# Kernel optimization log

Hardware: AMD Instinct MI355X
Metric: run time of the kernel (lower is better)

Reference implementation:

```python
import jax, jax.numpy as jnp
import numpy as np

B = 16
NS = [2048, 1024, 512, 256]
K = 12
GROUPS = 64
OUT = 1024
EPS = 1e-5


def setup_inputs() -> dict:
    key = jax.random.key(0)
    ks = iter(jax.random.split(key, 40))
    d = {}
    for i, n in enumerate(NS):
        d[f"fs{i}"] = jax.random.normal(next(ks), (B, n, 256), jnp.float32)
        d[f"xs{i}"] = jax.random.normal(next(ks), (B, n, 3), jnp.float32)
        ct = 1024 if i == 0 else 256
        d[f"ft{i}"] = jax.random.normal(next(ks), (B, n, ct), jnp.float32)
        d[f"xt{i}"] = jax.random.normal(next(ks), (B, n, 3), jnp.float32)
    d["Ws"] = jax.random.normal(next(ks), (4, OUT, 256), jnp.float32) * 0.05
    d["bWs"] = jax.random.normal(next(ks), (4, OUT), jnp.float32) * 0.05
    d["gs"] = jax.random.uniform(next(ks), (4, OUT), jnp.float32, 0.5, 1.5)
    d["bes"] = jax.random.normal(next(ks), (4, OUT), jnp.float32) * 0.05
    d["mus"] = jax.random.normal(next(ks), (4, OUT), jnp.float32) * 0.05
    d["vs"] = jax.random.uniform(next(ks), (4, OUT), jnp.float32, 0.5, 1.5)
    d["Wt0"] = jax.random.normal(next(ks), (OUT, 1024), jnp.float32) * 0.02
    d["Wt123"] = jax.random.normal(next(ks), (3, OUT, 256), jnp.float32) * 0.05
    d["bWt"] = jax.random.normal(next(ks), (4, OUT), jnp.float32) * 0.05
    d["gt"] = jax.random.uniform(next(ks), (4, OUT), jnp.float32, 0.5, 1.5)
    d["bet"] = jax.random.normal(next(ks), (4, OUT), jnp.float32) * 0.05
    d["mut"] = jax.random.normal(next(ks), (4, OUT), jnp.float32) * 0.05
    d["vt"] = jax.random.uniform(next(ks), (4, OUT), jnp.float32, 0.5, 1.5)
    return d


def fps(xyz, m):
    # furthest point sampling starting from index 0 (as in pointnet2_utils)
    b, n, _ = xyz.shape
    idxs = jnp.zeros((b, m), jnp.int32)
    d2 = jnp.full((b, n), 1e10, xyz.dtype)
    last = jnp.zeros((b,), jnp.int32)

    def body(i, st):
        idxs, d2, last = st
        lx = jnp.take_along_axis(xyz, last[:, None, None], axis=1)  # [b,1,3]
        d = jnp.sum((xyz - lx) ** 2, axis=-1)  # [b,n]
        d2 = jnp.minimum(d2, d)
        nxt = jnp.argmax(d2, axis=-1).astype(jnp.int32)
        return idxs.at[:, i].set(nxt), d2, nxt

    idxs, _, _ = jax.lax.fori_loop(1, m, body, (idxs, d2, last))
    return idxs


def gather_points(feat, idx):
    # feat [b,n,c], idx [b,...] -> [b,...,c]
    flat = idx.reshape(idx.shape[0], -1)
    out = jnp.take_along_axis(feat, flat[..., None], axis=1)
    return out.reshape(idx.shape + (feat.shape[-1],))


def knn_point(k, xyz, query):
    # squared pairwise distances [b,m,n]; k smallest (== torch.topk largest=False)
    d = (jnp.sum(query ** 2, -1, keepdims=True)
         - 2.0 * jnp.einsum('bmd,bnd->bmn', query, xyz)
         + jnp.sum(xyz ** 2, -1)[:, None, :])
    _, idx = jax.lax.top_k(-d, k)
    return idx.astype(jnp.int32)


def graph_op(grouped, w, b, g, be, mu, v):
    # grouped [B,M,K,C]; kernel-1 Conv1d == channel matmul; eval-mode BN; ReLU; max over K
    x = jnp.einsum('bmkc,oc->bmko', grouped, w) + b
    x = (x - mu) * (g * jax.lax.rsqrt(v + EPS)) + be
    x = jax.nn.relu(x)
    return jnp.max(x, axis=2)  # [B,M,O]


def reference(fs0, xs0, ft0, xt0, fs1, xs1, ft1, xt1, fs2, xs2, ft2, xt2,
              fs3, xs3, ft3, xt3, Ws, bWs, gs, bes, mus, vs,
              Wt0, Wt123, bWt, gt, bet, mut, vt):
    fs_list = [fs0, fs1, fs2, fs3]
    xs_list = [xs0, xs1, xs2, xs3]
    ft_list = [ft0, ft1, ft2, ft3]
    xt_list = [xt0, xt1, xt2, xt3]

    fps_idx = fps(xt_list[-1], GROUPS)              # [B,G]
    new_xyz = gather_points(xt_list[-1], fps_idx)   # [B,G,3]

    out_s, out_t = [], []
    for i in range(4):
        idx_t = knn_point(K, xt_list[i], new_xyz)   # [B,G,K]
        grp_t = gather_points(ft_list[i], idx_t)    # [B,G,K,Ct]
        idx_s = knn_point(K, xs_list[i], new_xyz)
        grp_s = gather_points(fs_list[i], idx_s)    # [B,G,K,256]
        wt = Wt0 if i == 0 else Wt123[i - 1]
        out_s.append(graph_op(grp_s, Ws[i], bWs[i], gs[i], bes[i], mus[i], vs[i]))
        out_t.append(graph_op(grp_t, wt, bWt[i], gt[i], bet[i], mut[i], vt[i]))
    return (tuple(out_s), tuple(out_t))
```

## Files before the change

kernel.cpp:

```cpp
#include <hip/hip_runtime.h>
#include <hip/hip_bf16.h>

#define DEVI __device__ __forceinline__

typedef __attribute__((ext_vector_type(8))) short bf16x8;
typedef __attribute__((ext_vector_type(4))) float f32x4;
typedef __attribute__((ext_vector_type(8))) unsigned short us8;
typedef __attribute__((ext_vector_type(4))) float fl4;

DEVI unsigned short f2bf(float f) {
  union { float f; unsigned u; } x; x.f = f;
  unsigned r = (x.u + 0x7fffu + ((x.u >> 16) & 1u)) >> 16;
  return (unsigned short)r;
}

DEVI float fadd3(float a, float b, float c) {
  return __fadd_rn(__fadd_rn(a, b), c);
}

__global__ __launch_bounds__(256) void prep_kernel(
    const float* __restrict__ Ws, const float* __restrict__ Wt0,
    const float* __restrict__ Wt123,
    const float* __restrict__ bWs, const float* __restrict__ gs,
    const float* __restrict__ bes, const float* __restrict__ mus,
    const float* __restrict__ vs,
    const float* __restrict__ bWt, const float* __restrict__ gt,
    const float* __restrict__ bet, const float* __restrict__ mut,
    const float* __restrict__ vt,
    char* __restrict__ wbf, float* __restrict__ bnA,
    float* __restrict__ bnB) {
  const unsigned id = blockIdx.x * 256u + threadIdx.x;
  const unsigned WN = 2883584u;
  if (id < WN) {
    float val; unsigned c, o, k, woffE;
    if (id < 1048576u) {
      c = id >> 18; unsigned rem = id & 262143u;
      o = rem >> 8; k = rem & 255u; val = Ws[id]; woffE = c << 18;
    } else if (id < 2097152u) {
      c = 4u; unsigned rem = id - 1048576u;
      o = rem >> 10; k = rem & 1023u; val = Wt0[rem]; woffE = 1048576u;
    } else {
      unsigned rem = id - 2097152u; unsigned cc = rem >> 18;
      c = 5u + cc; unsigned r2 = rem & 262143u;
      o = r2 >> 8; k = r2 & 255u; val = Wt123[rem];
      woffE = 2097152u + (cc << 18);
    }
    unsigned NKT = (c == 4u) ? 16u : 4u;
    unsigned ntile = o >> 8, op = o & 255u, kt = k >> 6, kl = k & 63u;
    unsigned byteoff = (woffE << 1) + ((ntile * NKT + kt) << 15) +
                       ((op * 128u + kl * 2u) ^ ((op & 7u) << 4));
    *(unsigned short*)(wbf + byteoff) = f2bf(val);
  } else if (id < WN + 8192u) {
    unsigned r = id - WN;
    unsigned c = r >> 10, o = r & 1023u;
    float g, bW, mu, v, be;
    if (c < 4u) { g = gs[r]; bW = bWs[r]; mu = mus[r]; v = vs[r]; be = bes[r]; }
    else {
      unsigned r2 = (c - 4u) * 1024u + o;
      g = gt[r2]; bW = bWt[r2]; mu = mut[r2]; v = vt[r2]; be = bet[r2];
    }
    float A = g / sqrtf(v + 1e-5f);
    float B = (bW - mu) * A + be;
    bnA[r] = A; bnB[r] = B;
  }
}

__global__ __launch_bounds__(64) void fps_kernel(const float* __restrict__ xt3,
                                                 float* __restrict__ newxyz) {
  const int b = blockIdx.x;
  const int t = threadIdx.x;
  const float* P = xt3 + (size_t)b * 256 * 3;
  float px[4], py[4], pz[4], d2[4];
#pragma unroll
  for (int j = 0; j < 4; ++j) {
    int p = t + 64 * j;
    px[j] = P[p * 3 + 0]; py[j] = P[p * 3 + 1]; pz[j] = P[p * 3 + 2];
    d2[j] = 1e10f;
  }
  float* NX = newxyz + (size_t)b * 64 * 3;
  float cx = __shfl(px[0], 0), cy = __shfl(py[0], 0), cz = __shfl(pz[0], 0);
  if (t == 0) { NX[0] = cx; NX[1] = cy; NX[2] = cz; }
  for (int i = 1; i < 64; ++i) {
    float bv = -1.0f; int bi = 0;
#pragma unroll
    for (int j = 0; j < 4; ++j) {
      float dx = __fsub_rn(px[j], cx), dy = __fsub_rn(py[j], cy),
            dz = __fsub_rn(pz[j], cz);
      float d = fadd3(__fmul_rn(dx, dx), __fmul_rn(dy, dy), __fmul_rn(dz, dz));
      d2[j] = fminf(d2[j], d);
      int p = t + 64 * j;
      if (j == 0) { bv = d2[0]; bi = t; }
      else if (d2[j] > bv) { bv = d2[j]; bi = p; }
    }
#pragma unroll
    for (int off = 32; off >= 1; off >>= 1) {
      float ov = __shfl_xor(bv, off);
      int oi = __shfl_xor(bi, off);
      if (ov > bv || (ov == bv && oi < bi)) { bv = ov; bi = oi; }
    }
    int s = bi;
    int owner = s & 63, slot = s >> 6;
    float sx = slot == 0 ? px[0] : slot == 1 ? px[1] : slot == 2 ? px[2] : px[3];
    float sy = slot == 0 ? py[0] : slot == 1 ? py[1] : slot == 2 ? py[2] : py[3];
    float sz = slot == 0 ? pz[0] : slot == 1 ? pz[1] : slot == 2 ? pz[2] : pz[3];
    cx = __shfl(sx, owner); cy = __shfl(sy, owner); cz = __shfl(sz, owner);
    if (t == 0) { NX[i * 3 + 0] = cx; NX[i * 3 + 1] = cy; NX[i * 3 + 2] = cz; }
  }
}

template <int NJ>
DEVI void knn_run(int lane, const float* __restrict__ X, float qx, float qy,
                  float qz, float qq, int* __restrict__ out) {
  float d2[NJ];
#pragma unroll
  for (int j = 0; j < NJ; ++j) {
    int pi = lane + 64 * j;
    float x = X[pi * 3 + 0], y = X[pi * 3 + 1], z = X[pi * 3 + 2];
    float xx = fadd3(__fmul_rn(x, x), __fmul_rn(y, y), __fmul_rn(z, z));
    float dot = fadd3(__fmul_rn(qx, x), __fmul_rn(qy, y), __fmul_rn(qz, z));
    d2[j] = __fadd_rn(__fsub_rn(qq, __fmul_rn(2.0f, dot)), xx);
  }
  for (int kk = 0; kk < 12; ++kk) {
    float bv = d2[0]; int bi = lane;
#pragma unroll
    for (int j = 1; j < NJ; ++j) {
      if (d2[j] < bv) { bv = d2[j]; bi = lane + 64 * j; }
    }
#pragma unroll
    for (int off = 1; off <= 32; off <<= 1) {
      float ov = __shfl_xor(bv, off);
      int oi = __shfl_xor(bi, off);
      if (ov < bv || (ov == bv && oi < bi)) { bv = ov; bi = oi; }
    }
    if (lane == 0) out[kk] = bi;
#pragma unroll
    for (int j = 0; j < NJ; ++j)
      if (bi == lane + 64 * j) d2[j] = 3.4e38f;
  }
}

struct KnnP { const float* xyz[8]; };

__global__ __launch_bounds__(256) void knn_kernel(KnnP p,
                                                  const float* __restrict__ newxyz,
                                                  int* __restrict__ idxbuf) {
  const int q = blockIdx.x * 4 + (threadIdx.x >> 6);
  const int lane = threadIdx.x & 63;
  const int c = q >> 10, b = (q >> 6) & 15, g = q & 63;
  const int n = 2048 >> (c & 3);
  const float* X = p.xyz[c] + (size_t)b * n * 3;
  const float* qp = newxyz + ((size_t)b * 64 + g) * 3;
  float qx = qp[0], qy = qp[1], qz = qp[2];
  float qq = fadd3(__fmul_rn(qx, qx), __fmul_rn(qy, qy), __fmul_rn(qz, qz));
  int* out = idxbuf + (size_t)q * 12;
  switch (c & 3) {
    case 0: knn_run<32>(lane, X, qx, qy, qz, qq, out); break;
    case 1: knn_run<16>(lane, X, qx, qy, qz, qq, out); break;
    case 2: knn_run<8>(lane, X, qx, qy, qz, qq, out); break;
    default: knn_run<4>(lane, X, qx, qy, qz, qq, out); break;
  }
}

struct GatherP {
  const float* feat[8];
  int n[8];
  unsigned base16[9];
  unsigned goffB[8];
  int lsh[8];
  int NKT[8];
};

__global__ __launch_bounds__(256) void gather_kernel(GatherP p,
                                                     const int* __restrict__ idxbuf,
                                                     char* __restrict__ grouped) {
  unsigned id = blockIdx.x * 256u + threadIdx.x;
  if (id >= p.base16[8]) return;
  int c = 0;
#pragma unroll
  for (int j = 1; j < 8; ++j) if (id >= p.base16[j]) c = j;
  unsigned local = id - p.base16[c];
  int lsh = p.lsh[c];
  unsigned r = local >> lsh;
  unsigned k8 = local & ((1u << lsh) - 1u);
  unsigned rowp = r & 255u, mtile = r >> 8, group = r >> 4, kslot = r & 15u;
  unsigned b = group >> 6;
  int ke = (kslot < 12u) ? (int)kslot : 0;
  int pidx = idxbuf[(size_t)c * 12288 + group * 12u + ke];
  int C = (lsh == 7) ? 1024 : 256;
  const float* src = p.feat[c] + ((size_t)b * p.n[c] + pidx) * C + k8 * 8u;
  fl4 v0 = *reinterpret_cast<const fl4*>(src);
  fl4 v1 = *reinterpret_cast<const fl4*>(src + 4);
  us8 ov;
  ov[0] = f2bf(v0[0]); ov[1] = f2bf(v0[1]); ov[2] = f2bf(v0[2]); ov[3] = f2bf(v0[3]);
  ov[4] = f2bf(v1[0]); ov[5] = f2bf(v1[1]); ov[6] = f2bf(v1[2]); ov[7] = f2bf(v1[3]);
  unsigned kt = k8 >> 3, kl8 = k8 & 7u;
  unsigned byteoff = p.goffB[c] + (mtile * (unsigned)p.NKT[c] + kt) * 32768u +
                     ((rowp * 128u + kl8 * 16u) ^ ((rowp & 7u) << 4));
  *reinterpret_cast<us8*>(grouped + byteoff) = ov;
}

struct GemmP {
  unsigned goff[8]; unsigned woff[8]; unsigned outoff[8];
  unsigned bnoff[8]; int K[8];
};

#define GLOAD_LDS16(gsrc, ldsdst)                                              \
  __builtin_amdgcn_global_load_lds(                                            \
      (const __attribute__((address_space(1))) void*)(gsrc),                   \
      (__attribute__((address_space(3))) void*)(ldsdst), 16, 0, 0)

template <int DBUF>
__global__ __launch_bounds__(512, 2) void gemm256_kernel(
    const unsigned short* __restrict__ grouped,
    const unsigned short* __restrict__ wbf, const float* __restrict__ bnA,
    const float* __restrict__ bnB, float* __restrict__ out, GemmP p) {
  extern __shared__ char smem[];
  const int z = blockIdx.z;
  const int NKT = p.K[z] >> 6;
  const char* Ag = (const char*)(grouped + p.goff[z]) +
                   (size_t)blockIdx.y * NKT * 32768;
  const char* Bg = (const char*)(wbf + p.woff[z]) +
                   (size_t)blockIdx.x * NKT * 32768;
  const int tid = threadIdx.x;
  const int lane = tid & 63, wid = tid >> 6;
  const int wr = wid >> 2, wc = wid & 3;

  f32x4 acc[8][4];
#pragma unroll
  for (int m = 0; m < 8; ++m)
#pragma unroll
    for (int n = 0; n < 4; ++n) acc[m][n] = (f32x4){0.f, 0.f, 0.f, 0.f};

  auto stage = [&](int buf, int kt2) {
    char* dstA = smem + buf * 65536;
    const char* srcA = Ag + (size_t)kt2 * 32768;
    const char* srcB = Bg + (size_t)kt2 * 32768;
#pragma unroll
    for (int it = 0; it < 4; ++it)
      GLOAD_LDS16(srcA + (it * 512 + tid) * 16, dstA + (it * 512 + wid * 64) * 16);
#pragma unroll
    for (int it = 0; it < 4; ++it)
      GLOAD_LDS16(srcB + (it * 512 + tid) * 16,
                  dstA + 32768 + (it * 512 + wid * 64) * 16);
  };

  auto compute = [&](int kt) {
    const char* As = smem + (DBUF ? ((kt & 1) * 65536) : 0);
    const char* Bs = As + 32768;
#pragma unroll
    for (int ks = 0; ks < 2; ++ks) {
      bf16x8 af[8], bv[4];
#pragma unroll
      for (int m = 0; m < 8; ++m) {
        int row = wr * 128 + m * 16 + (lane & 15);
        int byte = (row * 128 + ks * 64 + ((lane >> 4) * 16)) ^ ((lane & 7) << 4);
        af[m] = *reinterpret_cast<const bf16x8*>(As + byte);
      }
#pragma unroll
      for (int n = 0; n < 4; ++n) {
        int col = wc * 64 + n * 16 + (lane & 15);
        int byte = (col * 128 + ks * 64 + ((lane >> 4) * 16)) ^ ((lane & 7) << 4);
        bv[n] = *reinterpret_cast<const bf16x8*>(Bs + byte);
      }
#pragma unroll
      for (int m = 0; m < 8; ++m)
#pragma unroll
        for (int n = 0; n < 4; ++n)
          acc[m][n] = __builtin_amdgcn_mfma_f32_16x16x32_bf16(af[m], bv[n],
                                                              acc[m][n], 0, 0, 0);
    }
  };

  stage(0, 0);
  asm volatile("s_waitcnt vmcnt(0)" ::: "memory");
  __syncthreads();
  for (int kt = 0; kt < NKT; ++kt) {
    if (DBUF && kt + 1 < NKT) stage((kt + 1) & 1, kt + 1);
    compute(kt);
    if (DBUF) {
      if (kt + 1 < NKT) {
        asm volatile("s_waitcnt vmcnt(0)" ::: "memory");
        __syncthreads();
      }
    } else if (kt + 1 < NKT) {
      __syncthreads();
      stage(0, kt + 1);
      asm volatile("s_waitcnt vmcnt(0)" ::: "memory");
      __syncthreads();
    }
  }

  const float* bA = bnA + p.bnoff[z];
  const float* bB = bnB + p.bnoff[z];
  float* O = out + (size_t)p.outoff[z];
#pragma unroll
  for (int n = 0; n < 4; ++n) {
    int o = blockIdx.x * 256 + wc * 64 + n * 16 + (lane & 15);
    float sA = bA[o], sB = bB[o];
#pragma unroll
    for (int m = 0; m < 8; ++m) {
      float v = fmaxf(fmaxf(acc[m][n][0], acc[m][n][1]),
                      fmaxf(acc[m][n][2], acc[m][n][3]));
      v = fmaxf(v, __shfl_xor(v, 16));
      v = fmaxf(v, __shfl_xor(v, 32));
      if (lane < 16) {
        int group = blockIdx.y * 16 + wr * 8 + m;
        float val = fmaf(v, sA, sB);
        O[(size_t)group * 1024 + o] = fmaxf(val, 0.f);
      }
    }
  }
}

extern "C" void kernel_launch(void* const* d_in, const int* in_sizes, int n_in,
                              void* d_out, int out_size, void* d_ws,
                              size_t ws_size, hipStream_t stream) {
  (void)in_sizes; (void)n_in; (void)out_size; (void)ws_size;
  const float *fs[4], *xs[4], *ft[4], *xt[4];
  for (int i = 0; i < 4; ++i) {
    fs[i] = (const float*)d_in[4 * i + 0];
    xs[i] = (const float*)d_in[4 * i + 1];
    ft[i] = (const float*)d_in[4 * i + 2];
    xt[i] = (const float*)d_in[4 * i + 3];
  }
  const float* Ws = (const float*)d_in[16];
  const float* bWs = (const float*)d_in[17];
  const float* gs = (const float*)d_in[18];
  const float* bes = (const float*)d_in[19];
  const float* mus = (const float*)d_in[20];
  const float* vs = (const float*)d_in[21];
  const float* Wt0 = (const float*)d_in[22];
  const float* Wt123 = (const float*)d_in[23];
  const float* bWt = (const float*)d_in[24];
  const float* gt = (const float*)d_in[25];
  const float* bet = (const float*)d_in[26];
  const float* mut = (const float*)d_in[27];
  const float* vt = (const float*)d_in[28];

  char* ws = (char*)d_ws;
  float* newxyz = (float*)(ws + 0);
  int* idxbuf = (int*)(ws + 16384);
  float* bnA = (float*)(ws + 409600);
  float* bnB = (float*)(ws + 442368);
  char* wbf = ws + 475136;
  char* grouped = ws + 6242304;

  static const int NSarr[4] = {2048, 1024, 512, 256};
  const unsigned goff[8] = {0u,        4194304u,  8388608u,  12582912u,
                            16777216u, 33554432u, 37748736u, 41943040u};
  const unsigned woff[8] = {0u,       262144u,  524288u,  786432u,
                            1048576u, 2097152u, 2359296u, 2621440u};

  prep_kernel<<<11296, 256, 0, stream>>>(Ws, Wt0, Wt123, bWs, gs, bes, mus, vs,
                                         bWt, gt, bet, mut, vt, wbf, bnA, bnB);
  fps_kernel<<<16, 64, 0, stream>>>(xt[3], newxyz);

  KnnP kp;
  for (int i = 0; i < 4; ++i) {
    kp.xyz[i] = xs[i];
    kp.xyz[4 + i] = xt[i];
  }
  knn_kernel<<<2048, 256, 0, stream>>>(kp, newxyz, idxbuf);

  GatherP gp;
  unsigned cum = 0;
  for (int c = 0; c < 8; ++c) {
    int scale = c & 3;
    int K = (c == 4) ? 1024 : 256;
    gp.feat[c] = (c < 4) ? fs[scale] : ft[scale];
    gp.n[c] = NSarr[scale];
    gp.base16[c] = cum;
    gp.goffB[c] = goff[c] * 2u;
    gp.lsh[c] = (K == 1024) ? 7 : 5;
    gp.NKT[c] = K >> 6;
    cum += 16384u * (unsigned)(K / 8);
  }
  gp.base16[8] = cum;
  gather_kernel<<<(cum + 255u) / 256u, 256, 0, stream>>>(gp, idxbuf, grouped);

  GemmP mp;
  for (int c = 0; c < 8; ++c) {
    mp.goff[c] = goff[c]; mp.woff[c] = woff[c];
    mp.outoff[c] = (unsigned)c * 1048576u;
    mp.bnoff[c] = (unsigned)c * 1024u;
    mp.K[c] = (c == 4) ? 1024 : 256;
  }
  hipError_t attr_ok = hipFuncSetAttribute(
      (const void*)gemm256_kernel<1>,
      hipFuncAttributeMaxDynamicSharedMemorySize, 131072);
  if (attr_ok == hipSuccess) {
    gemm256_kernel<1><<<dim3(4, 64, 8), 512, 131072, stream>>>(
        (const unsigned short*)grouped, (const unsigned short*)wbf, bnA, bnB,
        (float*)d_out, mp);
  } else {
    gemm256_kernel<0><<<dim3(4, 64, 8), 512, 65536, stream>>>(
        (const unsigned short*)grouped, (const unsigned short*)wbf, bnA, bnB,
        (float*)d_out, mp);
  }
}
```

Before: 239.8 us.

## Restructure GEMM into 8-phase pipelined loop with prefetch-two and XCD block remap

```diff
diff --git a/kernel.cpp b/kernel.cpp
--- a/kernel.cpp
+++ b/kernel.cpp
@@ -209,8 +209,169 @@
       (const __attribute__((address_space(1))) void*)(gsrc),                   \
       (__attribute__((address_space(3))) void*)(ldsdst), 16, 0, 0)
 
-template <int DBUF>
-__global__ __launch_bounds__(512, 2) void gemm256_kernel(
+__global__ __launch_bounds__(512, 2) void gemm8p_kernel(
+    const unsigned short* __restrict__ grouped,
+    const unsigned short* __restrict__ wbf, const float* __restrict__ bnA,
+    const float* __restrict__ bnB, float* __restrict__ out, GemmP p) {
+  extern __shared__ char smem[];
+  const int bid = blockIdx.x;
+  const int logical = (bid & 7) * 256 + (bid >> 3);
+  const int z = logical >> 8;
+  const int rem = logical & 255;
+  const int mtile = rem >> 2, ntile = rem & 3;
+  const int NKT = p.K[z] >> 6;
+  const char* Ag = (const char*)(grouped + p.goff[z]) +
+                   (size_t)mtile * NKT * 32768;
+  const char* Bg = (const char*)(wbf + p.woff[z]) +
+                   (size_t)ntile * NKT * 32768;
+  const int tid = threadIdx.x;
+  const int lane = tid & 63, wid = tid >> 6;
+  const int wr = wid >> 2, wc = wid & 3;
+
+  const int hi16 = (lane >> 4) * 16;
+  const int swz = (lane & 7) << 4;
+  const int rowA = wr * 16384 + (lane & 15) * 128;
+  const int colB = wc * 8192 + (lane & 15) * 128;
+
+  f32x4 acc[8][4];
+#pragma unroll
+  for (int m = 0; m < 8; ++m)
+#pragma unroll
+    for (int n = 0; n < 4; ++n) acc[m][n] = (f32x4){0.f, 0.f, 0.f, 0.f};
+
+  auto stage = [&](int buf, int kt2) {
+    char* dst = smem + buf * 65536;
+    const char* sA = Ag + (size_t)kt2 * 32768;
+    const char* sB = Bg + (size_t)kt2 * 32768;
+#pragma unroll
+    for (int it = 0; it < 4; ++it)
+      GLOAD_LDS16(sA + (it * 512 + tid) * 16, dst + (it * 512 + wid * 64) * 16);
+#pragma unroll
+    for (int it = 0; it < 4; ++it)
+      GLOAD_LDS16(sB + (it * 512 + tid) * 16,
+                  dst + 32768 + (it * 512 + wid * 64) * 16);
+  };
+
+  stage(0, 0);
+  stage(1, 1);
+  asm volatile("s_waitcnt vmcnt(8)" ::: "memory");
+  __builtin_amdgcn_s_barrier();
+
+  for (int kt = 0; kt < NKT; ++kt) {
+    const char* As = smem + (kt & 1) * 65536;
+    const char* Bs = As + 32768;
+    bf16x8 af[4], bv[4];
+
+#pragma unroll
+    for (int j = 0; j < 4; ++j)
+      af[j] = *reinterpret_cast<const bf16x8*>(
+          As + ((rowA + j * 2048 + hi16) ^ swz));
+#pragma unroll
+    for (int n = 0; n < 4; ++n)
+      bv[n] = *reinterpret_cast<const bf16x8*>(
+          Bs + ((colB + n * 2048 + hi16) ^ swz));
+    __builtin_amdgcn_s_barrier();
+    asm volatile("s_waitcnt lgkmcnt(0)" ::: "memory");
+    __builtin_amdgcn_sched_barrier(0);
+    __builtin_amdgcn_s_setprio(1);
+#pragma unroll
+    for (int j = 0; j < 4; ++j)
+#pragma unroll
+      for (int n = 0; n < 4; ++n)
+        acc[j][n] = __builtin_amdgcn_mfma_f32_16x16x32_bf16(af[j], bv[n],
+                                                            acc[j][n], 0, 0, 0);
+    __builtin_amdgcn_s_setprio(0);
+    __builtin_amdgcn_s_barrier();
+
+#pragma unroll
+    for (int j = 0; j < 4; ++j)
+      af[j] = *reinterpret_cast<const bf16x8*>(
+          As + ((rowA + (4 + j) * 2048 + hi16) ^ swz));
+    __builtin_amdgcn_s_barrier();
+    asm volatile("s_waitcnt lgkmcnt(0)" ::: "memory");
+    __builtin_amdgcn_sched_barrier(0);
+    __builtin_amdgcn_s_setprio(1);
+#pragma unroll
+    for (int j = 0; j < 4; ++j)
+#pragma unroll
+      for (int n = 0; n < 4; ++n)
+        acc[4 + j][n] = __builtin_amdgcn_mfma_f32_16x16x32_bf16(
+            af[j], bv[n], acc[4 + j][n], 0, 0, 0);
+    __builtin_amdgcn_s_setprio(0);
+    __builtin_amdgcn_s_barrier();
+
+#pragma unroll
+    for (int j = 0; j < 4; ++j)
+      af[j] = *reinterpret_cast<const bf16x8*>(
+          As + ((rowA + j * 2048 + 64 + hi16) ^ swz));
+#pragma unroll
+    for (int n = 0; n < 4; ++n)
+      bv[n] = *reinterpret_cast<const bf16x8*>(
+          Bs + ((colB + n * 2048 + 64 + hi16) ^ swz));
+    __builtin_amdgcn_s_barrier();
+    asm volatile("s_waitcnt lgkmcnt(0)" ::: "memory");
+    __builtin_amdgcn_sched_barrier(0);
+    __builtin_amdgcn_s_setprio(1);
+#pragma unroll
+    for (int j = 0; j < 4; ++j)
+#pragma unroll
+      for (int n = 0; n < 4; ++n)
+        acc[j][n] = __builtin_amdgcn_mfma_f32_16x16x32_bf16(af[j], bv[n],
+                                                            acc[j][n], 0, 0, 0);
+    __builtin_amdgcn_s_setprio(0);
+    __builtin_amdgcn_s_barrier();
+
+#pragma unroll
+    for (int j = 0; j < 4; ++j)
+      af[j] = *reinterpret_cast<const bf16x8*>(
+          As + ((rowA + (4 + j) * 2048 + 64 + hi16) ^ swz));
+    __builtin_amdgcn_s_barrier();
+    asm volatile("s_waitcnt lgkmcnt(0)" ::: "memory");
+    __builtin_amdgcn_sched_barrier(0);
+    __builtin_amdgcn_s_setprio(1);
+#pragma unroll
+    for (int j = 0; j < 4; ++j)
+#pragma unroll
+      for (int n = 0; n < 4; ++n)
+        acc[4 + j][n] = __builtin_amdgcn_mfma_f32_16x16x32_bf16(
+            af[j], bv[n], acc[4 + j][n], 0, 0, 0);
+    __builtin_amdgcn_s_setprio(0);
+
+    const bool do_stage = (kt + 2 < NKT);
+    if (do_stage) stage(kt & 1, kt + 2);
+    if (kt + 1 < NKT) {
+      if (do_stage)
+        asm volatile("s_waitcnt vmcnt(8)" ::: "memory");
+      else
+        asm volatile("s_waitcnt vmcnt(0)" ::: "memory");
+    }
+    __builtin_amdgcn_sched_barrier(0);
+    __builtin_amdgcn_s_barrier();
+  }
+
+  const float* bA = bnA + p.bnoff[z];
+  const float* bB = bnB + p.bnoff[z];
+  float* O = out + (size_t)p.outoff[z];
+#pragma unroll
+  for (int n = 0; n < 4; ++n) {
+    int o = ntile * 256 + wc * 64 + n * 16 + (lane & 15);
+    float sA = bA[o], sB = bB[o];
+#pragma unroll
+    for (int m = 0; m < 8; ++m) {
+      float v = fmaxf(fmaxf(acc[m][n][0], acc[m][n][1]),
+                      fmaxf(acc[m][n][2], acc[m][n][3]));
+      v = fmaxf(v, __shfl_xor(v, 16));
+      v = fmaxf(v, __shfl_xor(v, 32));
+      if (lane < 16) {
+        int group = mtile * 16 + wr * 8 + m;
+        float val = fmaf(v, sA, sB);
+        O[(size_t)group * 1024 + o] = fmaxf(val, 0.f);
+      }
+    }
+  }
+}
+
+__global__ __launch_bounds__(512, 2) void gemm256_fb_kernel(
     const unsigned short* __restrict__ grouped,
     const unsigned short* __restrict__ wbf, const float* __restrict__ bnA,
     const float* __restrict__ bnB, float* __restrict__ out, GemmP p) {
@@ -231,22 +392,18 @@
 #pragma unroll
     for (int n = 0; n < 4; ++n) acc[m][n] = (f32x4){0.f, 0.f, 0.f, 0.f};
 
-  auto stage = [&](int buf, int kt2) {
-    char* dstA = smem + buf * 65536;
-    const char* srcA = Ag + (size_t)kt2 * 32768;
-    const char* srcB = Bg + (size_t)kt2 * 32768;
+  for (int kt = 0; kt < NKT; ++kt) {
+    const char* srcA = Ag + (size_t)kt * 32768;
+    const char* srcB = Bg + (size_t)kt * 32768;
 #pragma unroll
     for (int it = 0; it < 4; ++it)
-      GLOAD_LDS16(srcA + (it * 512 + tid) * 16, dstA + (it * 512 + wid * 64) * 16);
+      GLOAD_LDS16(srcA + (it * 512 + tid) * 16, smem + (it * 512 + wid * 64) * 16);
 #pragma unroll
     for (int it = 0; it < 4; ++it)
       GLOAD_LDS16(srcB + (it * 512 + tid) * 16,
-                  dstA + 32768 + (it * 512 + wid * 64) * 16);
-  };
-
-  auto compute = [&](int kt) {
-    const char* As = smem + (DBUF ? ((kt & 1) * 65536) : 0);
-    const char* Bs = As + 32768;
+                  smem + 32768 + (it * 512 + wid * 64) * 16);
+    asm volatile("s_waitcnt vmcnt(0)" ::: "memory");
+    __syncthreads();
 #pragma unroll
     for (int ks = 0; ks < 2; ++ks) {
       bf16x8 af[8], bv[4];
@@ -254,13 +411,13 @@
       for (int m = 0; m < 8; ++m) {
         int row = wr * 128 + m * 16 + (lane & 15);
         int byte = (row * 128 + ks * 64 + ((lane >> 4) * 16)) ^ ((lane & 7) << 4);
-        af[m] = *reinterpret_cast<const bf16x8*>(As + byte);
+        af[m] = *reinterpret_cast<const bf16x8*>(smem + byte);
       }
 #pragma unroll
       for (int n = 0; n < 4; ++n) {
         int col = wc * 64 + n * 16 + (lane & 15);
         int byte = (col * 128 + ks * 64 + ((lane >> 4) * 16)) ^ ((lane & 7) << 4);
-        bv[n] = *reinterpret_cast<const bf16x8*>(Bs + byte);
+        bv[n] = *reinterpret_cast<const bf16x8*>(smem + 32768 + byte);
       }
 #pragma unroll
       for (int m = 0; m < 8; ++m)
@@ -269,25 +426,7 @@
           acc[m][n] = __builtin_amdgcn_mfma_f32_16x16x32_bf16(af[m], bv[n],
                                                               acc[m][n], 0, 0, 0);
     }
-  };
-
-  stage(0, 0);
-  asm volatile("s_waitcnt vmcnt(0)" ::: "memory");
-  __syncthreads();
-  for (int kt = 0; kt < NKT; ++kt) {
-    if (DBUF && kt + 1 < NKT) stage((kt + 1) & 1, kt + 1);
-    compute(kt);
-    if (DBUF) {
-      if (kt + 1 < NKT) {
-        asm volatile("s_waitcnt vmcnt(0)" ::: "memory");
-        __syncthreads();
-      }
-    } else if (kt + 1 < NKT) {
-      __syncthreads();
-      stage(0, kt + 1);
-      asm volatile("s_waitcnt vmcnt(0)" ::: "memory");
-      __syncthreads();
-    }
+    __syncthreads();
   }
 
   const float* bA = bnA + p.bnoff[z];
@@ -386,14 +525,14 @@
     mp.K[c] = (c == 4) ? 1024 : 256;
   }
   hipError_t attr_ok = hipFuncSetAttribute(
-      (const void*)gemm256_kernel<1>,
+      (const void*)gemm8p_kernel,
       hipFuncAttributeMaxDynamicSharedMemorySize, 131072);
   if (attr_ok == hipSuccess) {
-    gemm256_kernel<1><<<dim3(4, 64, 8), 512, 131072, stream>>>(
+    gemm8p_kernel<<<2048, 512, 131072, stream>>>(
         (const unsigned short*)grouped, (const unsigned short*)wbf, bnA, bnB,
         (float*)d_out, mp);
   } else {
-    gemm256_kernel<0><<<dim3(4, 64, 8), 512, 65536, stream>>>(
+    gemm256_fb_kernel<<<dim3(4, 64, 8), 512, 65536, stream>>>(
         (const unsigned short*)grouped, (const unsigned short*)wbf, bnA, bnB,
         (float*)d_out, mp);
   }
```

Result: slower. 385.2 us (+60.6%).

## Fuse kNN feature gather into GEMM and read weights directly from global

Applied to the files above, without the earlier changes.

```diff
diff --git a/kernel.cpp b/kernel.cpp
--- a/kernel.cpp
+++ b/kernel.cpp
@@ -5,13 +5,19 @@
 
 typedef __attribute__((ext_vector_type(8))) short bf16x8;
 typedef __attribute__((ext_vector_type(4))) float f32x4;
-typedef __attribute__((ext_vector_type(8))) unsigned short us8;
 typedef __attribute__((ext_vector_type(4))) float fl4;
+typedef __attribute__((ext_vector_type(4))) unsigned int u32x4;
 
 DEVI unsigned short f2bf(float f) {
   union { float f; unsigned u; } x; x.f = f;
   unsigned r = (x.u + 0x7fffu + ((x.u >> 16) & 1u)) >> 16;
   return (unsigned short)r;
+}
+
+DEVI unsigned cvtpk(float lo, float hi) {
+  unsigned r;
+  asm("v_cvt_pk_bf16_f32 %0, %1, %2" : "=v"(r) : "v"(lo), "v"(hi));
+  return r;
 }
 
 DEVI float fadd3(float a, float b, float c) {
@@ -27,29 +33,16 @@
     const float* __restrict__ bWt, const float* __restrict__ gt,
     const float* __restrict__ bet, const float* __restrict__ mut,
     const float* __restrict__ vt,
-    char* __restrict__ wbf, float* __restrict__ bnA,
+    unsigned short* __restrict__ wlin, float* __restrict__ bnA,
     float* __restrict__ bnB) {
   const unsigned id = blockIdx.x * 256u + threadIdx.x;
   const unsigned WN = 2883584u;
   if (id < WN) {
-    float val; unsigned c, o, k, woffE;
-    if (id < 1048576u) {
-      c = id >> 18; unsigned rem = id & 262143u;
-      o = rem >> 8; k = rem & 255u; val = Ws[id]; woffE = c << 18;
-    } else if (id < 2097152u) {
-      c = 4u; unsigned rem = id - 1048576u;
-      o = rem >> 10; k = rem & 1023u; val = Wt0[rem]; woffE = 1048576u;
-    } else {
-      unsigned rem = id - 2097152u; unsigned cc = rem >> 18;
-      c = 5u + cc; unsigned r2 = rem & 262143u;
-      o = r2 >> 8; k = r2 & 255u; val = Wt123[rem];
-      woffE = 2097152u + (cc << 18);
-    }
-    unsigned NKT = (c == 4u) ? 16u : 4u;
-    unsigned ntile = o >> 8, op = o & 255u, kt = k >> 6, kl = k & 63u;
-    unsigned byteoff = (woffE << 1) + ((ntile * NKT + kt) << 15) +
-                       ((op * 128u + kl * 2u) ^ ((op & 7u) << 4));
-    *(unsigned short*)(wbf + byteoff) = f2bf(val);
+    float f;
+    if (id < 1048576u) f = Ws[id];
+    else if (id < 2097152u) f = Wt0[id - 1048576u];
+    else f = Wt123[id - 2097152u];
+    wlin[id] = f2bf(f);
   } else if (id < WN + 8192u) {
     unsigned r = id - WN;
     unsigned c = r >> 10, o = r & 1023u;
@@ -161,141 +154,133 @@
   }
 }
 
-struct GatherP {
+struct GemmFP {
   const float* feat[8];
+  unsigned woffE[8];
+  unsigned outoff[8];
+  int K[8];
   int n[8];
-  unsigned base16[9];
-  unsigned goffB[8];
-  int lsh[8];
-  int NKT[8];
 };
 
-__global__ __launch_bounds__(256) void gather_kernel(GatherP p,
-                                                     const int* __restrict__ idxbuf,
-                                                     char* __restrict__ grouped) {
-  unsigned id = blockIdx.x * 256u + threadIdx.x;
-  if (id >= p.base16[8]) return;
-  int c = 0;
-#pragma unroll
-  for (int j = 1; j < 8; ++j) if (id >= p.base16[j]) c = j;
-  unsigned local = id - p.base16[c];
-  int lsh = p.lsh[c];
-  unsigned r = local >> lsh;
-  unsigned k8 = local & ((1u << lsh) - 1u);
-  unsigned rowp = r & 255u, mtile = r >> 8, group = r >> 4, kslot = r & 15u;
-  unsigned b = group >> 6;
-  int ke = (kslot < 12u) ? (int)kslot : 0;
-  int pidx = idxbuf[(size_t)c * 12288 + group * 12u + ke];
-  int C = (lsh == 7) ? 1024 : 256;
-  const float* src = p.feat[c] + ((size_t)b * p.n[c] + pidx) * C + k8 * 8u;
-  fl4 v0 = *reinterpret_cast<const fl4*>(src);
-  fl4 v1 = *reinterpret_cast<const fl4*>(src + 4);
-  us8 ov;
-  ov[0] = f2bf(v0[0]); ov[1] = f2bf(v0[1]); ov[2] = f2bf(v0[2]); ov[3] = f2bf(v0[3]);
-  ov[4] = f2bf(v1[0]); ov[5] = f2bf(v1[1]); ov[6] = f2bf(v1[2]); ov[7] = f2bf(v1[3]);
-  unsigned kt = k8 >> 3, kl8 = k8 & 7u;
-  unsigned byteoff = p.goffB[c] + (mtile * (unsigned)p.NKT[c] + kt) * 32768u +
-                     ((rowp * 128u + kl8 * 16u) ^ ((rowp & 7u) << 4));
-  *reinterpret_cast<us8*>(grouped + byteoff) = ov;
-}
-
-struct GemmP {
-  unsigned goff[8]; unsigned woff[8]; unsigned outoff[8];
-  unsigned bnoff[8]; int K[8];
-};
-
-#define GLOAD_LDS16(gsrc, ldsdst)                                              \
-  __builtin_amdgcn_global_load_lds(                                            \
-      (const __attribute__((address_space(1))) void*)(gsrc),                   \
-      (__attribute__((address_space(3))) void*)(ldsdst), 16, 0, 0)
-
-template <int DBUF>
-__global__ __launch_bounds__(512, 2) void gemm256_kernel(
-    const unsigned short* __restrict__ grouped,
-    const unsigned short* __restrict__ wbf, const float* __restrict__ bnA,
-    const float* __restrict__ bnB, float* __restrict__ out, GemmP p) {
-  extern __shared__ char smem[];
-  const int z = blockIdx.z;
-  const int NKT = p.K[z] >> 6;
-  const char* Ag = (const char*)(grouped + p.goff[z]) +
-                   (size_t)blockIdx.y * NKT * 32768;
-  const char* Bg = (const char*)(wbf + p.woff[z]) +
-                   (size_t)blockIdx.x * NKT * 32768;
+__global__ __launch_bounds__(512, 2) void gemm_fused_kernel(
+    const unsigned short* __restrict__ wlin, const float* __restrict__ bnA,
+    const float* __restrict__ bnB, const int* __restrict__ idxbuf,
+    float* __restrict__ out, GemmFP p) {
+  __shared__ __align__(16) char smem[65536];
+  const int bid = blockIdx.x;
+  const int xcd = bid & 7;
+  const int tb = bid >> 3;
+  const int z = tb >> 5;
+  const int rem = (xcd << 5) | (tb & 31);
+  const int mtile = rem >> 2, ntile = rem & 3;
+  const int K = p.K[z];
+  const int NKT = K >> 6;
+  const int nPts = p.n[z];
+  const float* feat = p.feat[z];
+  const unsigned short* Bg = wlin + p.woffE[z];
+
   const int tid = threadIdx.x;
   const int lane = tid & 63, wid = tid >> 6;
   const int wr = wid >> 2, wc = wid & 3;
 
+  const int arow = tid >> 1;
+  const int ahalf = tid & 1;
+  int gl = arow >> 4;
+  int kslot = arow & 15;
+  int ke = (kslot < 12) ? kslot : 0;
+  int group = mtile * 16 + gl;
+  int pidx = idxbuf[z * 12288 + group * 12 + ke];
+  int bb = group >> 6;
+  const float* asrc = feat + ((size_t)bb * nPts + pidx) * K + ahalf * 32;
+  const unsigned awb = (unsigned)(arow * 128 + ahalf * 64);
+  const unsigned aswz = (unsigned)((arow & 7) << 4);
+
+  const int hi16 = (lane >> 4) * 16;
+  const int swz = (lane & 7) << 4;
+  const int rowA = wr * 16384 + (lane & 15) * 128;
+
+  const int koff = (lane >> 4) * 8;
+  unsigned colK[4];
+#pragma unroll
+  for (int n = 0; n < 4; ++n)
+    colK[n] = (unsigned)((ntile * 256 + wc * 64 + n * 16 + (lane & 15)) * K);
+
   f32x4 acc[8][4];
 #pragma unroll
   for (int m = 0; m < 8; ++m)
 #pragma unroll
     for (int n = 0; n < 4; ++n) acc[m][n] = (f32x4){0.f, 0.f, 0.f, 0.f};
 
-  auto stage = [&](int buf, int kt2) {
-    char* dstA = smem + buf * 65536;
-    const char* srcA = Ag + (size_t)kt2 * 32768;
-    const char* srcB = Bg + (size_t)kt2 * 32768;
-#pragma unroll
-    for (int it = 0; it < 4; ++it)
-      GLOAD_LDS16(srcA + (it * 512 + tid) * 16, dstA + (it * 512 + wid * 64) * 16);
-#pragma unroll
-    for (int it = 0; it < 4; ++it)
-      GLOAD_LDS16(srcB + (it * 512 + tid) * 16,
-                  dstA + 32768 + (it * 512 + wid * 64) * 16);
+  fl4 aH[8];
+  auto issueA = [&](int kt2) {
+    const fl4* s = (const fl4*)(asrc + kt2 * 64);
+#pragma unroll
+    for (int i = 0; i < 8; ++i) aH[i] = s[i];
   };
-
-  auto compute = [&](int kt) {
-    const char* As = smem + (DBUF ? ((kt & 1) * 65536) : 0);
-    const char* Bs = As + 32768;
+  auto writeA = [&](int buf) {
+    char* dst = smem + buf * 32768;
+#pragma unroll
+    for (int g = 0; g < 4; ++g) {
+      u32x4 w;
+      w[0] = cvtpk(aH[2 * g][0], aH[2 * g][1]);
+      w[1] = cvtpk(aH[2 * g][2], aH[2 * g][3]);
+      w[2] = cvtpk(aH[2 * g + 1][0], aH[2 * g + 1][1]);
+      w[3] = cvtpk(aH[2 * g + 1][2], aH[2 * g + 1][3]);
+      *(u32x4*)(dst + ((awb + g * 16u) ^ aswz)) = w;
+    }
+  };
+
+  issueA(0);
+  writeA(0);
+  if (NKT > 1) issueA(1);
+  __syncthreads();
+
+  for (int kt = 0; kt < NKT; ++kt) {
+    bf16x8 bv[2][4];
+#pragma unroll
+    for (int ks = 0; ks < 2; ++ks)
+#pragma unroll
+      for (int n = 0; n < 4; ++n)
+        bv[ks][n] = *(const bf16x8*)(Bg + colK[n] + kt * 64 + ks * 32 + koff);
+
+    if (kt + 1 < NKT) writeA((kt + 1) & 1);
+
+    const char* As = smem + (kt & 1) * 32768;
 #pragma unroll
     for (int ks = 0; ks < 2; ++ks) {
-      bf16x8 af[8], bv[4];
-#pragma unroll
-      for (int m = 0; m < 8; ++m) {
-        int row = wr * 128 + m * 16 + (lane & 15);
-        int byte = (row * 128 + ks * 64 + ((lane >> 4) * 16)) ^ ((lane & 7) << 4);
-        af[m] = *reinterpret_cast<const bf16x8*>(As + byte);
-      }
-#pragma unroll
-      for (int n = 0; n < 4; ++n) {
-        int col = wc * 64 + n * 16 + (lane & 15);
-        int byte = (col * 128 + ks * 64 + ((lane >> 4) * 16)) ^ ((lane & 7) << 4);
-        bv[n] = *reinterpret_cast<const bf16x8*>(Bs + byte);
-      }
-#pragma unroll
-      for (int m = 0; m < 8; ++m)
+      bf16x8 af[4];
+#pragma unroll
+      for (int j = 0; j < 4; ++j)
+        af[j] = *reinterpret_cast<const bf16x8*>(
+            As + ((rowA + j * 2048 + ks * 64 + hi16) ^ swz));
+#pragma unroll
+      for (int j = 0; j < 4; ++j)
 #pragma unroll
         for (int n = 0; n < 4; ++n)
-          acc[m][n] = __builtin_amdgcn_mfma_f32_16x16x32_bf16(af[m], bv[n],
-                                                              acc[m][n], 0, 0, 0);
-    }
-  };
-
-  stage(0, 0);
-  asm volatile("s_waitcnt vmcnt(0)" ::: "memory");
-  __syncthreads();
-  for (int kt = 0; kt < NKT; ++kt) {
-    if (DBUF && kt + 1 < NKT) stage((kt + 1) & 1, kt + 1);
-    compute(kt);
-    if (DBUF) {
-      if (kt + 1 < NKT) {
-        asm volatile("s_waitcnt vmcnt(0)" ::: "memory");
-        __syncthreads();
-      }
-    } else if (kt + 1 < NKT) {
-      __syncthreads();
-      stage(0, kt + 1);
-      asm volatile("s_waitcnt vmcnt(0)" ::: "memory");
-      __syncthreads();
-    }
-  }
-
-  const float* bA = bnA + p.bnoff[z];
-  const float* bB = bnB + p.bnoff[z];
+          acc[j][n] = __builtin_amdgcn_mfma_f32_16x16x32_bf16(
+              af[j], bv[ks][n], acc[j][n], 0, 0, 0);
+#pragma unroll
+      for (int j = 0; j < 4; ++j)
+        af[j] = *reinterpret_cast<const bf16x8*>(
+            As + ((rowA + (4 + j) * 2048 + ks * 64 + hi16) ^ swz));
+#pragma unroll
+      for (int j = 0; j < 4; ++j)
+#pragma unroll
+        for (int n = 0; n < 4; ++n)
+          acc[4 + j][n] = __builtin_amdgcn_mfma_f32_16x16x32_bf16(
+              af[j], bv[ks][n], acc[4 + j][n], 0, 0, 0);
+    }
+
+    if (kt + 2 < NKT) issueA(kt + 2);
+    __syncthreads();
+  }
+
+  const float* bA = bnA + (unsigned)z * 1024u;
+  const float* bB = bnB + (unsigned)z * 1024u;
   float* O = out + (size_t)p.outoff[z];
 #pragma unroll
   for (int n = 0; n < 4; ++n) {
-    int o = blockIdx.x * 256 + wc * 64 + n * 16 + (lane & 15);
+    int o = ntile * 256 + wc * 64 + n * 16 + (lane & 15);
     float sA = bA[o], sB = bB[o];
 #pragma unroll
     for (int m = 0; m < 8; ++m) {
@@ -304,9 +289,9 @@
       v = fmaxf(v, __shfl_xor(v, 16));
       v = fmaxf(v, __shfl_xor(v, 32));
       if (lane < 16) {
-        int group = blockIdx.y * 16 + wr * 8 + m;
+        int grp = mtile * 16 + wr * 8 + m;
         float val = fmaf(v, sA, sB);
-        O[(size_t)group * 1024 + o] = fmaxf(val, 0.f);
+        O[(size_t)grp * 1024 + o] = fmaxf(val, 0.f);
       }
     }
   }
@@ -342,17 +327,12 @@
   int* idxbuf = (int*)(ws + 16384);
   float* bnA = (float*)(ws + 409600);
   float* bnB = (float*)(ws + 442368);
-  char* wbf = ws + 475136;
-  char* grouped = ws + 6242304;
+  unsigned short* wlin = (unsigned short*)(ws + 475136);
 
   static const int NSarr[4] = {2048, 1024, 512, 256};
-  const unsigned goff[8] = {0u,        4194304u,  8388608u,  12582912u,
-                            16777216u, 33554432u, 37748736u, 41943040u};
-  const unsigned woff[8] = {0u,       262144u,  524288u,  786432u,
-                            1048576u, 2097152u, 2359296u, 2621440u};
 
   prep_kernel<<<11296, 256, 0, stream>>>(Ws, Wt0, Wt123, bWs, gs, bes, mus, vs,
-                                         bWt, gt, bet, mut, vt, wbf, bnA, bnB);
+                                         bWt, gt, bet, mut, vt, wlin, bnA, bnB);
   fps_kernel<<<16, 64, 0, stream>>>(xt[3], newxyz);
 
   KnnP kp;
@@ -362,39 +342,17 @@
   }
   knn_kernel<<<2048, 256, 0, stream>>>(kp, newxyz, idxbuf);
 
-  GatherP gp;
-  unsigned cum = 0;
+  GemmFP gp;
   for (int c = 0; c < 8; ++c) {
     int scale = c & 3;
-    int K = (c == 4) ? 1024 : 256;
     gp.feat[c] = (c < 4) ? fs[scale] : ft[scale];
     gp.n[c] = NSarr[scale];
-    gp.base16[c] = cum;
-    gp.goffB[c] = goff[c] * 2u;
-    gp.lsh[c] = (K == 1024) ? 7 : 5;
-    gp.NKT[c] = K >> 6;
-    cum += 16384u * (unsigned)(K / 8);
-  }
-  gp.base16[8] = cum;
-  gather_kernel<<<(cum + 255u) / 256u, 256, 0, stream>>>(gp, idxbuf, grouped);
-
-  GemmP mp;
-  for (int c = 0; c < 8; ++c) {
-    mp.goff[c] = goff[c]; mp.woff[c] = woff[c];
-    mp.outoff[c] = (unsigned)c * 1048576u;
-    mp.bnoff[c] = (unsigned)c * 1024u;
-    mp.K[c] = (c == 4) ? 1024 : 256;
-  }
-  hipError_t attr_ok = hipFuncSetAttribute(
-      (const void*)gemm256_kernel<1>,
-      hipFuncAttributeMaxDynamicSharedMemorySize, 131072);
-  if (attr_ok == hipSuccess) {
-    gemm256_kernel<1><<<dim3(4, 64, 8), 512, 131072, stream>>>(
-        (const unsigned short*)grouped, (const unsigned short*)wbf, bnA, bnB,
-        (float*)d_out, mp);
-  } else {
-    gemm256_kernel<0><<<dim3(4, 64, 8), 512, 65536, stream>>>(
-        (const unsigned short*)grouped, (const unsigned short*)wbf, bnA, bnB,
-        (float*)d_out, mp);
-  }
-}
+    gp.K[c] = (c == 4) ? 1024 : 256;
+    gp.outoff[c] = (unsigned)c * 1048576u;
+    gp.woffE[c] = (c < 4)   ? (unsigned)c * 262144u
+                 : (c == 4) ? 1048576u
+                            : 2097152u + (unsigned)(c - 5) * 262144u;
+  }
+  gemm_fused_kernel<<<2048, 512, 0, stream>>>(wlin, bnA, bnB, idxbuf,
+                                              (float*)d_out, gp);
+}
```

Result: slower. 279.4 us (+16.5%).
